# Kernel tuning notes

Measured on AMD Instinct MI355X. Metric: run time of the kernel, lower is better.

Reference implementation:

```python
import jax, jax.numpy as jnp
import numpy as np

B, CIN, COUT, HID, K, H, W = 16, 512, 512, 512, 3, 64, 64

def setup_inputs() -> dict:
    key = jax.random.key(0)
    ks = jax.random.split(key, 8)
    x = jax.random.normal(ks[0], (B, CIN, H, W), dtype=jnp.float32)
    y = jax.random.normal(ks[1], (B, HID), dtype=jnp.float32)
    noise = jax.random.normal(ks[2], (B, 1, H, W), dtype=jnp.float32)
    # params (lrmul=1): weight ~ N(0,1)/sqrt(lrmul), bias zeros
    weight = jax.random.normal(ks[3], (COUT, CIN, K, K), dtype=jnp.float32)
    bias = jnp.zeros((1, COUT, 1, 1), dtype=jnp.float32)
    # ScaleLinear (equalized-lr linear): raw weight ~ N(0,1), runtime scale 1/sqrt(fan_in)
    mod_w = jax.random.normal(ks[4], (CIN, HID), dtype=jnp.float32)
    mod_b = jnp.zeros((CIN,), dtype=jnp.float32)
    noise_scale = jnp.zeros((1,), dtype=jnp.float32)
    return {"x": x, "y": y, "noise": noise, "weight": weight, "bias": bias,
            "mod_w": mod_w, "mod_b": mod_b, "noise_scale": noise_scale}

def reference(x, y, noise, weight, bias, mod_w, mod_b, noise_scale):
    O, I, k, _ = weight.shape
    runtime_coef = 1.0 / np.sqrt(I * k * k)  # gain=1, lrmul=1
    w = weight * runtime_coef                # shared scaled weight [O,I,k,k]
    # style modulation: s = mod(y) + 1, equalized-lr linear scale 1/sqrt(hidden)
    mod_scale = 1.0 / np.sqrt(mod_w.shape[1])
    s = y @ (mod_w.T * mod_scale) + mod_b + 1.0   # [B, I]
    # demodulation coeff without materializing per-sample weights:
    # d[b,o] = rsqrt(sum_{i,kx,ky} (w[o,i]*s[b,i])^2 + eps)
    w2 = jnp.sum(w * w, axis=(2, 3))              # [O, I]
    d = jax.lax.rsqrt(jnp.einsum('oi,bi->bo', w2, s * s) + 1e-8)  # [B, O]
    # fold modulation into input scale, demod into output scale (StyleGAN2 trick;
    # mathematically identical to grouped conv with per-sample weights)
    xm = x * s[:, :, None, None]
    out = jax.lax.conv_general_dilated(
        xm, w, window_strides=(1, 1), padding=((1, 1), (1, 1)),
        dimension_numbers=('NCHW', 'OIHW', 'NCHW'))
    out = out * d[:, :, None, None]
    out = out + noise * noise_scale   # noisy=True, explicit noise input
    out = out + bias                  # lrmul=1
    return out
```

## Files before the change

kernel.cpp:

```cpp
#include <hip/hip_runtime.h>
#include <hip/hip_bf16.h>

typedef unsigned short ushortT;
typedef __attribute__((ext_vector_type(8))) short short8;
typedef __attribute__((ext_vector_type(4))) float f32x4;

#define CIN 512
#define COUTC 512
#define HIDC 512
#define BATCH 16
#define HDIM 64
#define WDIM 64
#define HP 66


__device__ __forceinline__ unsigned short f2bf(float f) {
    __hip_bfloat16 h = __float2bfloat16(f);
    return __builtin_bit_cast(unsigned short, h);
}

__device__ __forceinline__ void gload16(const ushortT* g, ushortT* l) {
    __builtin_amdgcn_global_load_lds(
        (const __attribute__((address_space(1))) void*)g,
        (__attribute__((address_space(3))) void*)l, 16, 0, 0);
}

__global__ void k_style(const float* __restrict__ y, const float* __restrict__ mw,
                        const float* __restrict__ mb, float* __restrict__ s) {
    int lane = threadIdx.x & 63;
    int wid = blockIdx.x * 4 + (threadIdx.x >> 6);
    int b = wid >> 9, i = wid & 511;
    int h0 = lane * 8;
    float4 ya = *(const float4*)(y + b * HIDC + h0);
    float4 yb = *(const float4*)(y + b * HIDC + h0 + 4);
    float4 wa = *(const float4*)(mw + (size_t)i * HIDC + h0);
    float4 wb = *(const float4*)(mw + (size_t)i * HIDC + h0 + 4);
    float v = ya.x*wa.x + ya.y*wa.y + ya.z*wa.z + ya.w*wa.w
            + yb.x*wb.x + yb.y*wb.y + yb.z*wb.z + yb.w*wb.w;
    #pragma unroll
    for (int off = 32; off > 0; off >>= 1) v += __shfl_down(v, off);
    if (lane == 0) s[wid] = v * 0.04419417382415922f + mb[i] + 1.0f;
}

__global__ void k_prepw(const float* __restrict__ w, float* __restrict__ w2,
                        ushortT* __restrict__ wbt) {
    int t = blockIdx.x * 256 + threadIdx.x;
    const float* wp = w + (size_t)t * 9;
    const float coef = 0.014731391274719739f;
    float sum = 0.f;
    #pragma unroll
    for (int k = 0; k < 9; ++k) {
        float v = wp[k] * coef;
        sum += v * v;
        wbt[(size_t)k * (COUTC * CIN) + t] = f2bf(v);
    }
    w2[t] = sum;
}

__global__ void k_demod(const float* __restrict__ w2, const float* __restrict__ s,
                        float* __restrict__ d) {
    int lane = threadIdx.x & 63;
    int wid = blockIdx.x * 4 + (threadIdx.x >> 6);
    int b = wid >> 9, o = wid & 511;
    int i0 = lane * 8;
    float4 wa = *(const float4*)(w2 + (size_t)o * CIN + i0);
    float4 wb = *(const float4*)(w2 + (size_t)o * CIN + i0 + 4);
    float4 sa = *(const float4*)(s + b * CIN + i0);
    float4 sb = *(const float4*)(s + b * CIN + i0 + 4);
    float v = wa.x*sa.x*sa.x + wa.y*sa.y*sa.y + wa.z*sa.z*sa.z + wa.w*sa.w*sa.w
            + wb.x*sb.x*sb.x + wb.y*sb.y*sb.y + wb.z*sb.z*sb.z + wb.w*sb.w*sb.w;
    #pragma unroll
    for (int off = 32; off > 0; off >>= 1) v += __shfl_down(v, off);
    if (lane == 0) d[wid] = rsqrtf(v + 1e-8f);
}

__global__ void k_pad(const float* __restrict__ x, const float* __restrict__ s,
                      ushortT* __restrict__ xpad) {
    __shared__ float tilef[64 * 33];
    int bid = blockIdx.x;
    int cchunk = bid & 15;
    int rem = bid >> 4;
    int prow = rem % HP;
    int b = rem / HP;
    int tid = threadIdx.x;
    size_t rowbase = (((size_t)b * HP + prow) * HP) * CIN + cchunk * 32;
    if (prow == 0 || prow == HP - 1) {
        short8 z = {};
        for (int q = tid; q < HP * 4; q += 256) {
            int col = q >> 2, sub = q & 3;
            *(short8*)(xpad + rowbase + (size_t)col * CIN + sub * 8) = z;
        }
        return;
    }
    int xr = prow - 1;
    int u = tid & 15;
    #pragma unroll
    for (int cl = 0; cl < 32; cl += 16) {
        int c = cl + (tid >> 4);
        float4 v = *(const float4*)(x + (((size_t)b * CIN + cchunk * 32 + c) * HDIM + xr) * WDIM + u * 4);
        float sv = s[b * CIN + cchunk * 32 + c];
        tilef[(u * 4 + 0) * 33 + c] = v.x * sv;
        tilef[(u * 4 + 1) * 33 + c] = v.y * sv;
        tilef[(u * 4 + 2) * 33 + c] = v.z * sv;
        tilef[(u * 4 + 3) * 33 + c] = v.w * sv;
    }
    __syncthreads();
    int col = 1 + (tid >> 2), sub = tid & 3;
    const float* tr = tilef + (col - 1) * 33 + sub * 8;
    short8 o;
    #pragma unroll
    for (int r = 0; r < 8; ++r) o[r] = (short)f2bf(tr[r]);
    *(short8*)(xpad + rowbase + (size_t)col * CIN + sub * 8) = o;
    if (tid < 8) {
        short8 z = {};
        int bcol = (tid < 4) ? 0 : (HP - 1);
        *(short8*)(xpad + rowbase + (size_t)bcol * CIN + (tid & 3) * 8) = z;
    }
}

#define MFMA_CLUSTER(MH) do { \
    __builtin_amdgcn_s_setprio(1); \
    _Pragma("unroll") for (int m_ = 0; m_ < 4; ++m_) { \
        _Pragma("unroll") for (int n_ = 0; n_ < 4; ++n_) \
            acc[(MH)*4 + m_][n_] = __builtin_amdgcn_mfma_f32_16x16x32_bf16( \
                af[m_], bf[n_], acc[(MH)*4 + m_][n_], 0, 0, 0); } \
    __builtin_amdgcn_s_setprio(0); \
} while (0)

#define DS_A(MH, KH) do { \
    _Pragma("unroll") for (int m_ = 0; m_ < 4; ++m_) { \
        int row_ = wave_m * 128 + (MH)*64 + m_*16 + l15; \
        af[m_] = *(const short8*)(Ar + row_*64 + ((((KH)*4 + quad) ^ (row_ & 7)) * 8)); \
    } } while (0)

#define DS_B(KH) do { \
    _Pragma("unroll") for (int n_ = 0; n_ < 4; ++n_) { \
        int row_ = wave_n * 64 + n_*16 + l15; \
        bf[n_] = *(const short8*)(Br + row_*64 + ((((KH)*4 + quad) ^ (row_ & 7)) * 8)); \
    } } while (0)

__global__ __launch_bounds__(512, 2) void k_conv(
    const ushortT* __restrict__ wbt, const ushortT* __restrict__ xpad,
    const float* __restrict__ dcoef, const float* __restrict__ bias,
    const float* __restrict__ noise, const float* __restrict__ nscp,
    float* __restrict__ out)
{
    extern __shared__ __align__(16) ushortT smem[];

    int tid = threadIdx.x;
    int lane = tid & 63;
    int wave = tid >> 6;
    int wave_m = wave >> 2;
    int wave_n = wave & 3;
    int l15 = lane & 15;
    int quad = lane >> 4;

    int bid = blockIdx.x;
    int wg = (bid & 7) * 64 + (bid >> 3);
    int mtile = wg >> 8;
    int ntile = wg & 255;
    int b = ntile >> 4;
    int h0 = (ntile & 15) << 2;
    int cout0 = mtile << 8;

    unsigned aoff[4], boff[4], dstE[4];
    #pragma unroll
    for (int ca = 0; ca < 4; ++ca) {
        int a = ca * 512 + tid;
        int row = a >> 3;
        int sub = (a & 7) ^ (row & 7);
        aoff[ca] = (unsigned)((cout0 + row) * CIN + sub * 8);
        int prow = row >> 6;
        int pcol = row & 63;
        boff[ca] = (unsigned)((((b * HP) + h0 + prow) * HP + pcol) * CIN + sub * 8);
        dstE[ca] = (unsigned)(ca * 4096 + wave * 512);
    }

    f32x4 acc[8][4] = {};

    {
        const ushortT* Asrc = wbt;
        const ushortT* Bsrc = xpad;
        #pragma unroll
        for (int ca = 0; ca < 4; ++ca) {
            gload16(Asrc + aoff[ca], smem + dstE[ca]);
            gload16(Bsrc + boff[ca], smem + 32768 + dstE[ca]);
        }
        asm volatile("s_waitcnt vmcnt(0)");
        __builtin_amdgcn_s_barrier();
    }

    #pragma unroll 2
    for (int ks = 0; ks < 72; ++ks) {
        int cur = ks & 1;
        const ushortT* Ar = smem + cur * 16384;
        const ushortT* Br = smem + 32768 + cur * 16384;
        ushortT* Aw = smem + (cur ^ 1) * 16384;
        ushortT* Bw = smem + 32768 + (cur ^ 1) * 16384;
        int ksn = ks + 1;
        bool st = ksn < 72;
        int tn = ksn >> 3, ccn = ksn & 7;
        const ushortT* Asrc = wbt + tn * (COUTC * CIN) + ccn * 64;
        const ushortT* Bsrc = xpad + ((tn / 3) * HP + (tn % 3)) * CIN + ccn * 64;

        short8 af[4], bf[4];

        if (st) {
            gload16(Asrc + aoff[0], Aw + dstE[0]); gload16(Bsrc + boff[0], Bw + dstE[0]);
            gload16(Asrc + aoff[1], Aw + dstE[1]); gload16(Bsrc + boff[1], Bw + dstE[1]);
        }
        DS_B(0);
        DS_A(0, 0);
        __builtin_amdgcn_s_barrier();
        asm volatile("s_waitcnt lgkmcnt(0)");
        MFMA_CLUSTER(0);
        __builtin_amdgcn_s_barrier();

        if (st) {
            gload16(Asrc + aoff[2], Aw + dstE[2]); gload16(Bsrc + boff[2], Bw + dstE[2]);
            gload16(Asrc + aoff[3], Aw + dstE[3]); gload16(Bsrc + boff[3], Bw + dstE[3]);
        }
        DS_A(1, 0);
        __builtin_amdgcn_s_barrier();
        asm volatile("s_waitcnt lgkmcnt(0)");
        MFMA_CLUSTER(1);
        __builtin_amdgcn_s_barrier();

        DS_B(1);
        DS_A(0, 1);
        __builtin_amdgcn_s_barrier();
        asm volatile("s_waitcnt lgkmcnt(0)");
        MFMA_CLUSTER(0);
        __builtin_amdgcn_s_barrier();

        DS_A(1, 1);
        __builtin_amdgcn_s_barrier();
        asm volatile("s_waitcnt lgkmcnt(0)");
        MFMA_CLUSTER(1);
        if (st) asm volatile("s_waitcnt vmcnt(0)");
        __builtin_amdgcn_s_barrier();
    }

    float ns = nscp[0];
    int col = lane & 15, rq = lane >> 4;
    #pragma unroll
    for (int nj = 0; nj < 4; ++nj) {
        int pos = wave_n * 64 + nj * 16 + col;
        int hh = h0 + (pos >> 6), ww = pos & 63;
        float nz = noise[((size_t)b << 12) + (hh << 6) + ww] * ns;
        #pragma unroll
        for (int mi = 0; mi < 8; ++mi) {
            int coutb = cout0 + wave_m * 128 + mi * 16 + rq * 4;
            f32x4 dv = *(const f32x4*)(dcoef + b * COUTC + coutb);
            f32x4 bv = *(const f32x4*)(bias + coutb);
            f32x4 a = acc[mi][nj];
            #pragma unroll
            for (int r = 0; r < 4; ++r) {
                out[(((size_t)(b * COUTC + coutb + r)) << 12) + (hh << 6) + ww]
                    = a[r] * dv[r] + nz + bv[r];
            }
        }
    }
}

extern "C" void kernel_launch(void* const* d_in, const int* in_sizes, int n_in,
                              void* d_out, int out_size, void* d_ws, size_t ws_size,
                              hipStream_t stream) {
    const float* x      = (const float*)d_in[0];
    const float* y      = (const float*)d_in[1];
    const float* noise  = (const float*)d_in[2];
    const float* weight = (const float*)d_in[3];
    const float* bias   = (const float*)d_in[4];
    const float* mod_w  = (const float*)d_in[5];
    const float* mod_b  = (const float*)d_in[6];
    const float* nsc    = (const float*)d_in[7];
    float* out = (float*)d_out;

    char* ws = (char*)d_ws;
    float*   s     = (float*)(ws);
    float*   dcoef = (float*)(ws + 32768);
    float*   w2    = (float*)(ws + 65536);
    ushortT* wbt   = (ushortT*)(ws + 1114112);
    ushortT* xpad  = (ushortT*)(ws + 5832704);

    static bool attr_done = false;
    if (!attr_done) {
        (void)hipFuncSetAttribute(reinterpret_cast<const void*>(k_conv),
                                  hipFuncAttributeMaxDynamicSharedMemorySize, 131072);
        attr_done = true;
    }

    k_style<<<dim3(2048), dim3(256), 0, stream>>>(y, mod_w, mod_b, s);
    k_prepw<<<dim3(1024), dim3(256), 0, stream>>>(weight, w2, wbt);
    k_demod<<<dim3(2048), dim3(256), 0, stream>>>(w2, s, dcoef);
    k_pad<<<dim3(BATCH * HP * 16), dim3(256), 0, stream>>>(x, s, xpad);
    k_conv<<<dim3(512), dim3(512), 131072, stream>>>(wbt, xpad, dcoef, bias, noise, nsc, out);
}
```

Baseline: 529.6 us.

## Double-buffer LDS fragment registers and drop per-cluster barriers in conv main loop

Fragment reads from LDS now use two register sets (P/Q). Each MFMA cluster therefore runs while the next cluster's A/B fragments are being read, instead of waiting on lgkmcnt(0) first. Most per-cluster s_barrier calls are gone, leaving one wait plus barrier per k-step, after which the first fragments of the next buffer are prefetched. The cost is higher register pressure from the extra short8 arrays under launch_bounds(512,2). Correctness now rests on compiler-inserted LDS waits and a single barrier per k-step.

Result: slower. 777.4 us (+46.8%).

```diff
diff --git a/kernel.cpp b/kernel.cpp
--- a/kernel.cpp
+++ b/kernel.cpp
@@ -118,26 +118,28 @@
     }
 }
 
-#define MFMA_CLUSTER(MH) do { \
+#define RD_A(dst, MH, KH, Abase) do { \
+    _Pragma("unroll") for (int m_ = 0; m_ < 4; ++m_) { \
+        int row_ = wave_m * 128 + (MH)*64 + m_*16 + l15; \
+        dst[m_] = *(const short8*)((Abase) + row_*64 + ((((KH)*4 + quad) ^ (row_ & 7)) * 8)); \
+    } } while (0)
+
+#define RD_B(dst, KH, Bbase) do { \
+    _Pragma("unroll") for (int n_ = 0; n_ < 4; ++n_) { \
+        int row_ = wave_n * 64 + n_*16 + l15; \
+        dst[n_] = *(const short8*)((Bbase) + row_*64 + ((((KH)*4 + quad) ^ (row_ & 7)) * 8)); \
+    } } while (0)
+
+#define CLUSTER(MH, A_, B_) do { \
     __builtin_amdgcn_s_setprio(1); \
     _Pragma("unroll") for (int m_ = 0; m_ < 4; ++m_) { \
         _Pragma("unroll") for (int n_ = 0; n_ < 4; ++n_) \
             acc[(MH)*4 + m_][n_] = __builtin_amdgcn_mfma_f32_16x16x32_bf16( \
-                af[m_], bf[n_], acc[(MH)*4 + m_][n_], 0, 0, 0); } \
+                A_[m_], B_[n_], acc[(MH)*4 + m_][n_], 0, 0, 0); } \
     __builtin_amdgcn_s_setprio(0); \
 } while (0)
 
-#define DS_A(MH, KH) do { \
-    _Pragma("unroll") for (int m_ = 0; m_ < 4; ++m_) { \
-        int row_ = wave_m * 128 + (MH)*64 + m_*16 + l15; \
-        af[m_] = *(const short8*)(Ar + row_*64 + ((((KH)*4 + quad) ^ (row_ & 7)) * 8)); \
-    } } while (0)
-
-#define DS_B(KH) do { \
-    _Pragma("unroll") for (int n_ = 0; n_ < 4; ++n_) { \
-        int row_ = wave_n * 64 + n_*16 + l15; \
-        bf[n_] = *(const short8*)(Br + row_*64 + ((((KH)*4 + quad) ^ (row_ & 7)) * 8)); \
-    } } while (0)
+#define BAR() do { __builtin_amdgcn_s_barrier(); asm volatile("" ::: "memory"); } while (0)
 
 __global__ __launch_bounds__(512, 2) void k_conv(
     const ushortT* __restrict__ wbt, const ushortT* __restrict__ xpad,
@@ -177,6 +179,7 @@
     }
 
     f32x4 acc[8][4] = {};
+    short8 aP[4], aQ[4], bP[4], bQ[4];
 
     {
         const ushortT* Asrc = wbt;
@@ -186,8 +189,10 @@
             gload16(Asrc + aoff[ca], smem + dstE[ca]);
             gload16(Bsrc + boff[ca], smem + 32768 + dstE[ca]);
         }
-        asm volatile("s_waitcnt vmcnt(0)");
-        __builtin_amdgcn_s_barrier();
+        asm volatile("s_waitcnt vmcnt(0)" ::: "memory");
+        BAR();
+        RD_A(aP, 0, 0, smem);
+        RD_B(bP, 0, smem + 32768);
     }
 
     #pragma unroll 2
@@ -203,42 +208,32 @@
         const ushortT* Asrc = wbt + tn * (COUTC * CIN) + ccn * 64;
         const ushortT* Bsrc = xpad + ((tn / 3) * HP + (tn % 3)) * CIN + ccn * 64;
 
-        short8 af[4], bf[4];
-
         if (st) {
             gload16(Asrc + aoff[0], Aw + dstE[0]); gload16(Bsrc + boff[0], Bw + dstE[0]);
             gload16(Asrc + aoff[1], Aw + dstE[1]); gload16(Bsrc + boff[1], Bw + dstE[1]);
         }
-        DS_B(0);
-        DS_A(0, 0);
-        __builtin_amdgcn_s_barrier();
-        asm volatile("s_waitcnt lgkmcnt(0)");
-        MFMA_CLUSTER(0);
-        __builtin_amdgcn_s_barrier();
+        RD_A(aQ, 1, 0, Ar);
+        CLUSTER(0, aP, bP);
 
         if (st) {
             gload16(Asrc + aoff[2], Aw + dstE[2]); gload16(Bsrc + boff[2], Bw + dstE[2]);
             gload16(Asrc + aoff[3], Aw + dstE[3]); gload16(Bsrc + boff[3], Bw + dstE[3]);
         }
-        DS_A(1, 0);
-        __builtin_amdgcn_s_barrier();
-        asm volatile("s_waitcnt lgkmcnt(0)");
-        MFMA_CLUSTER(1);
-        __builtin_amdgcn_s_barrier();
-
-        DS_B(1);
-        DS_A(0, 1);
-        __builtin_amdgcn_s_barrier();
-        asm volatile("s_waitcnt lgkmcnt(0)");
-        MFMA_CLUSTER(0);
-        __builtin_amdgcn_s_barrier();
-
-        DS_A(1, 1);
-        __builtin_amdgcn_s_barrier();
-        asm volatile("s_waitcnt lgkmcnt(0)");
-        MFMA_CLUSTER(1);
-        if (st) asm volatile("s_waitcnt vmcnt(0)");
-        __builtin_amdgcn_s_barrier();
+        RD_A(aP, 0, 1, Ar);
+        RD_B(bQ, 1, Br);
+        CLUSTER(1, aQ, bP);
+
+        RD_A(aQ, 1, 1, Ar);
+        CLUSTER(0, aP, bQ);
+
+        if (st) {
+            asm volatile("s_waitcnt vmcnt(0)" ::: "memory");
+            BAR();
+            RD_A(aP, 0, 0, Aw);
+            RD_B(bP, 0, Bw);
+        }
+        CLUSTER(1, aQ, bQ);
+        BAR();
     }
 
     float ns = nscp[0];
```
